# Performance work log

Hardware: AMD Instinct MI355X
Metric: run time of the kernel (lower is better)

The kernel has to match this reference:

```python
import jax, jax.numpy as jnp
import numpy as np

N_ITERS = 1000  # hardcoded in the original module
EPS = 1e-6


def setup_inputs() -> dict:
    key = jax.random.key(0)
    k1, k2 = jax.random.split(key)
    embeds = jax.random.normal(k1, (30000, 64), dtype=jnp.float32)
    # torch does t.rand(...) inside forward; we hoist it here for determinism
    init_centroids = jax.random.uniform(k2, (500, 64), dtype=jnp.float32)
    return {"embeds": embeds, "init_centroids": init_centroids}


def reference(embeds, init_centroids):
    N, D = embeds.shape
    K = init_centroids.shape[0]
    # ||e||^2 is loop-invariant; squared L2 distance expanded as
    # ||e||^2 - 2 e.c + ||c||^2 (same math as (e-c)^2.sum(-1), no [N,K,D] blowup)
    e_sq = jnp.sum(embeds * embeds, axis=1)  # [N]
    ones = jnp.ones((N, 1), dtype=embeds.dtype)

    def step(carry, _):
        cents, _, _ = carry
        c_sq = jnp.sum(cents * cents, axis=1)  # [K]
        dists = e_sq[:, None] - 2.0 * (embeds @ cents.T) + c_sq[None, :]  # [N,K]
        idxs = jnp.argmin(dists, axis=1)  # [N] int32
        sums = jax.ops.segment_sum(embeds, idxs, num_segments=K)  # [K,D]
        counts = jax.ops.segment_sum(ones, idxs, num_segments=K)  # [K,1]
        new_cents = sums / (counts + EPS)
        return (new_cents, idxs, counts), None

    init = (init_centroids,
            jnp.zeros((N,), dtype=jnp.int32),
            jnp.zeros((K, 1), dtype=embeds.dtype))
    (centroids, idxs, clust_nums), _ = jax.lax.scan(step, init, None, length=N_ITERS)
    return centroids, idxs, clust_nums
```

## Files before the change

kernel.cpp:

```cpp
#include <hip/hip_runtime.h>
#include <math.h>

#define N_PTS   30000
#define DIM     64
#define K_C     500
#define K_PAD   512
#define N_ITERS 1000

#define TM    128
#define NTM   235
#define GRID  NTM
#define BLK   1024

#define FPSCALE 262144.0f
#define INV_FPSCALE (1.0 / 262144.0)

#define BAR_STRIDE 32
#define BAR_REL_OFF (GRID * BAR_STRIDE)

__device__ __forceinline__ int SLOT(int i) { return (i / 12) * K_PAD + 500 + (i % 12); }
#define MLS(i)  SLOT(i)
#define CNT_ML  SLOT(128)

__device__ __forceinline__ void gridbar(int* bar, int n) {
  __syncthreads();
  if (blockIdx.x == 0) {
    const int t = threadIdx.x;
    if (t >= 1 && t < GRID) {
      while (__hip_atomic_load(&bar[t * BAR_STRIDE], __ATOMIC_RELAXED,
                               __HIP_MEMORY_SCOPE_AGENT) < n)
        __builtin_amdgcn_s_sleep(2);
      __builtin_amdgcn_fence(__ATOMIC_ACQUIRE, "agent");
    }
    __syncthreads();
    if (t == 0)
      __hip_atomic_store(&bar[BAR_REL_OFF], n, __ATOMIC_RELEASE,
                         __HIP_MEMORY_SCOPE_AGENT);
  } else {
    if (threadIdx.x == 0) {
      __hip_atomic_store(&bar[blockIdx.x * BAR_STRIDE], n, __ATOMIC_RELEASE,
                         __HIP_MEMORY_SCOPE_AGENT);
      while (__hip_atomic_load(&bar[BAR_REL_OFF], __ATOMIC_RELAXED,
                               __HIP_MEMORY_SCOPE_AGENT) < n)
        __builtin_amdgcn_s_sleep(2);
      __builtin_amdgcn_fence(__ATOMIC_ACQUIRE, "agent");
    }
    __syncthreads();
  }
}

__global__ __launch_bounds__(BLK)
void k_persist(const float* __restrict__ embeds,
               const float* __restrict__ cents0,
               float* __restrict__ esq,
               int* __restrict__ idx,
               int* __restrict__ gcnt,
               unsigned long long* __restrict__ acc,
               int* mov,
               float* __restrict__ csq_g,
               int* __restrict__ changed,
               int* __restrict__ bar,
               float* __restrict__ out) {
  __shared__ __align__(16) float As[DIM * TM];
  __shared__ __align__(16) float Bs[DIM * K_PAD];
  int* BsI = (int*)Bs;
  const int tid = threadIdx.x;
  const int bid = blockIdx.x;
  int bno = 0;

  {
    const int w = bid * 16 + (tid >> 6), d = tid & 63;
    for (int p = w; p < N_PTS; p += GRID * 16) {
      float v = embeds[(size_t)p * DIM + d];
      float s = v * v;
      #pragma unroll
      for (int m = 1; m < 64; m <<= 1) s += __shfl_xor(s, m, 64);
      if (d == 0) esq[p] = s;
    }
  }
  gridbar(bar, ++bno);

  const int m0 = bid * TM;
  const int tx = tid & 63, ty = tid >> 6;

  #pragma unroll
  for (int l = 0; l < 2; ++l) {
    int e = tid + l * BLK;
    int pl = e & 127, d4 = e >> 7;
    int p = m0 + pl;
    float4 v = make_float4(0.f, 0.f, 0.f, 0.f);
    if (p < N_PTS) v = *reinterpret_cast<const float4*>(embeds + (size_t)p * DIM + d4 * 4);
    As[(d4 * 4 + 0) * TM + pl] = v.x; As[(d4 * 4 + 1) * TM + pl] = v.y;
    As[(d4 * 4 + 2) * TM + pl] = v.z; As[(d4 * 4 + 3) * TM + pl] = v.w;
  }
  float esq_r[8];
  #pragma unroll
  for (int i = 0; i < 8; ++i) {
    int p = m0 + ty * 8 + i;
    esq_r[i] = (p < N_PTS) ? esq[p] : 0.f;
  }

  for (int it = 0; it < N_ITERS; ++it) {
    if (tid == 0) BsI[CNT_ML] = 0;

    if (tid < K_PAD) {
      bool doStage;
      if (it == 0)      doStage = true;
      else if (it == 1) doStage = (tid < K_C);
      else              doStage = (tid < K_C) && (mov[tid] >= it - 1);
      if (doStage) {
        float s4[16];
        if (it == 0) {
          if (tid < K_C) {
            #pragma unroll
            for (int l = 0; l < 16; ++l) {
              float4 v = *reinterpret_cast<const float4*>(cents0 + (size_t)tid * DIM + l * 4);
              Bs[(l * 4 + 0) * K_PAD + tid] = v.x; Bs[(l * 4 + 1) * K_PAD + tid] = v.y;
              Bs[(l * 4 + 2) * K_PAD + tid] = v.z; Bs[(l * 4 + 3) * K_PAD + tid] = v.w;
              s4[l] = (v.x * v.x + v.y * v.y) + (v.z * v.z + v.w * v.w);
            }
          } else {
            #pragma unroll
            for (int l = 0; l < 16; ++l) {
              Bs[(l * 4 + 0) * K_PAD + tid] = 0.f; Bs[(l * 4 + 1) * K_PAD + tid] = 0.f;
              Bs[(l * 4 + 2) * K_PAD + tid] = 0.f; Bs[(l * 4 + 3) * K_PAD + tid] = 0.f;
              s4[l] = 0.f;
            }
          }
        } else {
          float fc = (float)gcnt[tid] + 1e-6f;
          #pragma unroll
          for (int l = 0; l < 16; ++l) {
            const unsigned long long* ap = acc + (size_t)tid * DIM + l * 4;
            longlong2 a0 = *reinterpret_cast<const longlong2*>(ap);
            longlong2 a1 = *reinterpret_cast<const longlong2*>(ap + 2);
            float n0 = (float)((double)a0.x * INV_FPSCALE) / fc;
            float n1 = (float)((double)a0.y * INV_FPSCALE) / fc;
            float n2 = (float)((double)a1.x * INV_FPSCALE) / fc;
            float n3 = (float)((double)a1.y * INV_FPSCALE) / fc;
            Bs[(l * 4 + 0) * K_PAD + tid] = n0; Bs[(l * 4 + 1) * K_PAD + tid] = n1;
            Bs[(l * 4 + 2) * K_PAD + tid] = n2; Bs[(l * 4 + 3) * K_PAD + tid] = n3;
            s4[l] = (n0 * n0 + n1 * n1) + (n2 * n2 + n3 * n3);
          }
        }
        float s8[8], s16[4], s32[2];
        #pragma unroll
        for (int m = 0; m < 8; ++m) s8[m] = s4[2 * m] + s4[2 * m + 1];
        #pragma unroll
        for (int m = 0; m < 4; ++m) s16[m] = s8[2 * m] + s8[2 * m + 1];
        s32[0] = s16[0] + s16[1]; s32[1] = s16[2] + s16[3];
        float cs = s32[0] + s32[1];
        csq_g[tid] = (tid < K_C) ? cs : INFINITY;
      }
    }
    __syncthreads();

    float acc_r[8][8];
    #pragma unroll
    for (int i = 0; i < 8; ++i)
      #pragma unroll
      for (int j = 0; j < 8; ++j) acc_r[i][j] = 0.f;

    #pragma unroll 4
    for (int d = 0; d < DIM; ++d) {
      const float* ar = As + d * TM + ty * 8;
      float4 a0 = *reinterpret_cast<const float4*>(ar);
      float4 a1 = *reinterpret_cast<const float4*>(ar + 4);
      const float* br = Bs + d * K_PAD + tx * 4;
      float4 b0 = *reinterpret_cast<const float4*>(br);
      float4 b1 = *reinterpret_cast<const float4*>(br + 256);
      float av[8] = {a0.x, a0.y, a0.z, a0.w, a1.x, a1.y, a1.z, a1.w};
      float bv[8] = {b0.x, b0.y, b0.z, b0.w, b1.x, b1.y, b1.z, b1.w};
      #pragma unroll
      for (int i = 0; i < 8; ++i)
        #pragma unroll
        for (int j = 0; j < 8; ++j)
          acc_r[i][j] = fmaf(av[i], bv[j], acc_r[i][j]);
    }

    float4 c0 = *reinterpret_cast<const float4*>(csq_g + tx * 4);
    float4 c1 = *reinterpret_cast<const float4*>(csq_g + 256 + tx * 4);
    float cv[8] = {c0.x, c0.y, c0.z, c0.w, c1.x, c1.y, c1.z, c1.w};
    float best[8]; int bidx[8];
    #pragma unroll
    for (int i = 0; i < 8; ++i) { best[i] = INFINITY; bidx[i] = 0; }
    #pragma unroll
    for (int g = 0; g < 2; ++g) {
      #pragma unroll
      for (int j = 0; j < 4; ++j) {
        int c = g * 4 + j;
        int n = g * 256 + tx * 4 + j;
        #pragma unroll
        for (int i = 0; i < 8; ++i) {
          float dd = (esq_r[i] - 2.0f * acc_r[i][c]) + cv[c];
          if (dd < best[i]) { best[i] = dd; bidx[i] = n; }
        }
      }
    }

    #pragma unroll
    for (int i = 0; i < 8; ++i) {
      float v = best[i]; int bi = bidx[i];
      #pragma unroll
      for (int s = 1; s < 64; s <<= 1) {
        float ov = __shfl_xor(v, s, 64);
        int   oi = __shfl_xor(bi, s, 64);
        if (ov < v || (ov == v && oi < bi)) { v = ov; bi = oi; }
      }
      if (tx == 0) {
        int pl = ty * 8 + i, p = m0 + pl;
        if (p < N_PTS) {
          int old = idx[p];
          if (old != bi) {
            idx[p] = bi;
            int slot = atomicAdd(&BsI[CNT_ML], 1);
            BsI[MLS(slot)] = pl | ((old + 1) << 7) | (bi << 16);
            if (slot == 0)
              __hip_atomic_store(&changed[it], 1, __ATOMIC_RELAXED,
                                 __HIP_MEMORY_SCOPE_AGENT);
          }
        }
      }
    }
    __syncthreads();

    {
      const int w8 = tid >> 6, lane = tid & 63;
      const int cnt = BsI[CNT_ML];
      for (int i = w8; i < cnt; i += 16) {
        int e = BsI[MLS(i)];
        int pl = e & 127, old = ((e >> 7) & 511) - 1, k = e >> 16;
        float v = embeds[(size_t)(m0 + pl) * DIM + lane];
        long long iv = (long long)__float2int_rn(v * FPSCALE);
        atomicAdd(&acc[(size_t)k * DIM + lane], (unsigned long long)iv);
        if (old >= 0)
          atomicAdd(&acc[(size_t)old * DIM + lane], (unsigned long long)(-iv));
        if (lane == 0) {
          atomicAdd(&gcnt[k], 1);
          __hip_atomic_store(&mov[k], it, __ATOMIC_RELAXED, __HIP_MEMORY_SCOPE_AGENT);
          if (old >= 0) {
            atomicAdd(&gcnt[old], -1);
            __hip_atomic_store(&mov[old], it, __ATOMIC_RELAXED, __HIP_MEMORY_SCOPE_AGENT);
          }
        }
      }
    }
    gridbar(bar, ++bno);

    if (__hip_atomic_load(&changed[it], __ATOMIC_RELAXED,
                          __HIP_MEMORY_SCOPE_AGENT) == 0)
      break;
  }

  const int tot = K_C * DIM + N_PTS + K_C;
  for (int g = bid * BLK + tid; g < tot; g += GRID * BLK) {
    float v;
    if (g < K_C * DIM) {
      int k = g >> 6;
      v = (float)((double)(long long)acc[g] * INV_FPSCALE) / ((float)gcnt[k] + 1e-6f);
    } else if (g < K_C * DIM + N_PTS) {
      v = (float)idx[g - K_C * DIM];
    } else {
      v = (float)gcnt[g - K_C * DIM - N_PTS];
    }
    out[g] = v;
  }
}

extern "C" void kernel_launch(void* const* d_in, const int* in_sizes, int n_in,
                              void* d_out, int out_size, void* d_ws, size_t ws_size,
                              hipStream_t stream) {
  const float* embeds = (const float*)d_in[0];
  const float* init_c = (const float*)d_in[1];
  float* out = (float*)d_out;

  char* w = (char*)d_ws;
  size_t off = 0;
  auto alloc = [&](size_t bytes) -> void* {
    void* p = w + off;
    off += (bytes + 255) & ~(size_t)255;
    return p;
  };
  float* cents0 = (float*)alloc((size_t)K_C * DIM * sizeof(float));
  float* esq    = (float*)alloc((size_t)N_PTS * sizeof(float));
  int*   idx    = (int*)  alloc((size_t)N_PTS * sizeof(int));
  int*   gcnt   = (int*)  alloc((size_t)K_C * sizeof(int));
  unsigned long long* acc =
      (unsigned long long*)alloc((size_t)K_C * DIM * sizeof(unsigned long long));
  int*   mov    = (int*)  alloc((size_t)K_PAD * sizeof(int));
  float* csq_g  = (float*)alloc((size_t)K_PAD * sizeof(float));
  int*   chg    = (int*)  alloc((size_t)N_ITERS * sizeof(int));
  int*   bar    = (int*)  alloc((size_t)(BAR_REL_OFF + 64) * sizeof(int));

  hipMemcpyAsync(cents0, init_c, (size_t)K_C * DIM * sizeof(float),
                 hipMemcpyDeviceToDevice, stream);
  hipMemsetAsync(gcnt, 0, (size_t)K_C * sizeof(int), stream);
  hipMemsetAsync(acc, 0, (size_t)K_C * DIM * sizeof(unsigned long long), stream);
  hipMemsetAsync(idx, 0xFF, (size_t)N_PTS * sizeof(int), stream);
  hipMemsetAsync(mov, 0xFF, (size_t)K_PAD * sizeof(int), stream);
  hipMemsetAsync(chg, 0, (size_t)N_ITERS * sizeof(int), stream);
  hipMemsetAsync(bar, 0, (size_t)(BAR_REL_OFF + 64) * sizeof(int), stream);

  k_persist<<<dim3(GRID), dim3(BLK), 0, stream>>>(
      embeds, cents0, esq, idx, gcnt, acc, mov, csq_g, chg, bar, out);
}
```

Measured before the change: 1.951 ms.

## Halve block size, split centroid GEMM into two halves with register prefetch

```diff
diff --git a/kernel.cpp b/kernel.cpp
--- a/kernel.cpp
+++ b/kernel.cpp
@@ -10,7 +10,7 @@
 #define TM    128
 #define NTM   235
 #define GRID  NTM
-#define BLK   1024
+#define BLK   512
 
 #define FPSCALE 262144.0f
 #define INV_FPSCALE (1.0 / 262144.0)
@@ -69,8 +69,8 @@
   int bno = 0;
 
   {
-    const int w = bid * 16 + (tid >> 6), d = tid & 63;
-    for (int p = w; p < N_PTS; p += GRID * 16) {
+    const int w = bid * 8 + (tid >> 6), d = tid & 63;
+    for (int p = w; p < N_PTS; p += GRID * 8) {
       float v = embeds[(size_t)p * DIM + d];
       float s = v * v;
       #pragma unroll
@@ -81,10 +81,10 @@
   gridbar(bar, ++bno);
 
   const int m0 = bid * TM;
-  const int tx = tid & 63, ty = tid >> 6;
+  const int tx = tid & 31, ty = tid >> 5;
 
   #pragma unroll
-  for (int l = 0; l < 2; ++l) {
+  for (int l = 0; l < 4; ++l) {
     int e = tid + l * BLK;
     int pl = e & 127, d4 = e >> 7;
     int p = m0 + pl;
@@ -93,17 +93,11 @@
     As[(d4 * 4 + 0) * TM + pl] = v.x; As[(d4 * 4 + 1) * TM + pl] = v.y;
     As[(d4 * 4 + 2) * TM + pl] = v.z; As[(d4 * 4 + 3) * TM + pl] = v.w;
   }
-  float esq_r[8];
-  #pragma unroll
-  for (int i = 0; i < 8; ++i) {
-    int p = m0 + ty * 8 + i;
-    esq_r[i] = (p < N_PTS) ? esq[p] : 0.f;
-  }
 
   for (int it = 0; it < N_ITERS; ++it) {
     if (tid == 0) BsI[CNT_ML] = 0;
 
-    if (tid < K_PAD) {
+    {
       bool doStage;
       if (it == 0)      doStage = true;
       else if (it == 1) doStage = (tid < K_C);
@@ -155,45 +149,66 @@
     }
     __syncthreads();
 
-    float acc_r[8][8];
-    #pragma unroll
-    for (int i = 0; i < 8; ++i)
-      #pragma unroll
-      for (int j = 0; j < 8; ++j) acc_r[i][j] = 0.f;
-
-    #pragma unroll 4
-    for (int d = 0; d < DIM; ++d) {
-      const float* ar = As + d * TM + ty * 8;
-      float4 a0 = *reinterpret_cast<const float4*>(ar);
-      float4 a1 = *reinterpret_cast<const float4*>(ar + 4);
-      const float* br = Bs + d * K_PAD + tx * 4;
-      float4 b0 = *reinterpret_cast<const float4*>(br);
-      float4 b1 = *reinterpret_cast<const float4*>(br + 256);
-      float av[8] = {a0.x, a0.y, a0.z, a0.w, a1.x, a1.y, a1.z, a1.w};
-      float bv[8] = {b0.x, b0.y, b0.z, b0.w, b1.x, b1.y, b1.z, b1.w};
-      #pragma unroll
-      for (int i = 0; i < 8; ++i)
-        #pragma unroll
-        for (int j = 0; j < 8; ++j)
-          acc_r[i][j] = fmaf(av[i], bv[j], acc_r[i][j]);
-    }
-
-    float4 c0 = *reinterpret_cast<const float4*>(csq_g + tx * 4);
-    float4 c1 = *reinterpret_cast<const float4*>(csq_g + 256 + tx * 4);
-    float cv[8] = {c0.x, c0.y, c0.z, c0.w, c1.x, c1.y, c1.z, c1.w};
     float best[8]; int bidx[8];
     #pragma unroll
     for (int i = 0; i < 8; ++i) { best[i] = INFINITY; bidx[i] = 0; }
+
     #pragma unroll
-    for (int g = 0; g < 2; ++g) {
-      #pragma unroll
-      for (int j = 0; j < 4; ++j) {
-        int c = g * 4 + j;
-        int n = g * 256 + tx * 4 + j;
-        #pragma unroll
-        for (int i = 0; i < 8; ++i) {
-          float dd = (esq_r[i] - 2.0f * acc_r[i][c]) + cv[c];
-          if (dd < best[i]) { best[i] = dd; bidx[i] = n; }
+    for (int h = 0; h < 2; ++h) {
+      const float* ap = As + ty * 8;
+      const float* bp = Bs + h * 256 + tx * 4;
+
+      float acc_r[8][8];
+      #pragma unroll
+      for (int i = 0; i < 8; ++i)
+        #pragma unroll
+        for (int j = 0; j < 8; ++j) acc_r[i][j] = 0.f;
+
+      float4 a0 = *reinterpret_cast<const float4*>(ap);
+      float4 a1 = *reinterpret_cast<const float4*>(ap + 4);
+      float4 b0 = *reinterpret_cast<const float4*>(bp);
+      float4 b1 = *reinterpret_cast<const float4*>(bp + 128);
+
+      #pragma unroll 8
+      for (int d = 0; d < DIM; ++d) {
+        const int dn = (d + 1 < DIM) ? d + 1 : d;
+        float4 na0 = *reinterpret_cast<const float4*>(ap + dn * TM);
+        float4 na1 = *reinterpret_cast<const float4*>(ap + dn * TM + 4);
+        float4 nb0 = *reinterpret_cast<const float4*>(bp + dn * K_PAD);
+        float4 nb1 = *reinterpret_cast<const float4*>(bp + dn * K_PAD + 128);
+
+        float av[8] = {a0.x, a0.y, a0.z, a0.w, a1.x, a1.y, a1.z, a1.w};
+        float bv[8] = {b0.x, b0.y, b0.z, b0.w, b1.x, b1.y, b1.z, b1.w};
+        #pragma unroll
+        for (int i = 0; i < 8; ++i)
+          #pragma unroll
+          for (int j = 0; j < 8; ++j)
+            acc_r[i][j] = fmaf(av[i], bv[j], acc_r[i][j]);
+
+        a0 = na0; a1 = na1; b0 = nb0; b1 = nb1;
+      }
+
+      float esq_h[8];
+      #pragma unroll
+      for (int i = 0; i < 8; ++i) {
+        int p = m0 + ty * 8 + i;
+        esq_h[i] = (p < N_PTS) ? esq[p] : 0.f;
+      }
+      const int nbase = h * 256;
+      float4 c0 = *reinterpret_cast<const float4*>(csq_g + nbase + tx * 4);
+      float4 c1 = *reinterpret_cast<const float4*>(csq_g + nbase + 128 + tx * 4);
+      float cv[8] = {c0.x, c0.y, c0.z, c0.w, c1.x, c1.y, c1.z, c1.w};
+      #pragma unroll
+      for (int g = 0; g < 2; ++g) {
+        #pragma unroll
+        for (int j = 0; j < 4; ++j) {
+          int c = g * 4 + j;
+          int n = nbase + g * 128 + tx * 4 + j;
+          #pragma unroll
+          for (int i = 0; i < 8; ++i) {
+            float dd = (esq_h[i] - 2.0f * acc_r[i][c]) + cv[c];
+            if (dd < best[i]) { best[i] = dd; bidx[i] = n; }
+          }
         }
       }
     }
@@ -202,7 +217,7 @@
     for (int i = 0; i < 8; ++i) {
       float v = best[i]; int bi = bidx[i];
       #pragma unroll
-      for (int s = 1; s < 64; s <<= 1) {
+      for (int s = 1; s < 32; s <<= 1) {
         float ov = __shfl_xor(v, s, 64);
         int   oi = __shfl_xor(bi, s, 64);
         if (ov < v || (ov == v && oi < bi)) { v = ov; bi = oi; }
@@ -227,7 +242,7 @@
     {
       const int w8 = tid >> 6, lane = tid & 63;
       const int cnt = BsI[CNT_ML];
-      for (int i = w8; i < cnt; i += 16) {
+      for (int i = w8; i < cnt; i += 8) {
         int e = BsI[MLS(i)];
         int pl = e & 127, old = ((e >> 7) & 511) - 1, k = e >> 16;
         float v = embeds[(size_t)(m0 + pl) * DIM + lane];
```

Measured after the change: 1.903 ms, median of 2. 1.03x faster.
